# Performance work log

Hardware: AMD Instinct MI355X
Metric: run time of the kernel (lower is better)

## Reference

```python
import math
import jax, jax.numpy as jnp
import numpy as np

N_NODES = 50_000
N_EDGES = 500_000
INPUT_DIM = 6
HIDDEN = 128
FREQS = 32
LN_EPS = 1e-5
TWO_PI = 2.0 * math.pi


def wrap_angle(a):
    return (a + math.pi) % (2.0 * math.pi) - math.pi


def setup_inputs() -> dict:
    key = jax.random.key(0)
    ks = jax.random.split(key, 12)
    source = jax.random.normal(ks[0], (N_NODES, 5), dtype=jnp.float32)
    target = jax.random.normal(ks[1], (N_NODES, 5), dtype=jnp.float32)
    edge = jax.random.randint(ks[2], (2, N_EDGES), 0, N_NODES, dtype=jnp.int64)
    K = 2 * FREQS + 1
    # FourierEmbedding params: freqs table + 6 per-dim MLPs (Linear->LN->ReLU->Linear), stacked over dim axis
    freqs = jax.random.normal(ks[3], (INPUT_DIM, FREQS), dtype=jnp.float32)
    W1 = jax.random.normal(ks[4], (INPUT_DIM, K, HIDDEN), dtype=jnp.float32) * (1.0 / math.sqrt(K))
    b1 = jnp.zeros((INPUT_DIM, HIDDEN), dtype=jnp.float32)
    ln_w = jnp.ones((INPUT_DIM, HIDDEN), dtype=jnp.float32)
    ln_b = jnp.zeros((INPUT_DIM, HIDDEN), dtype=jnp.float32)
    W2 = jax.random.normal(ks[5], (INPUT_DIM, HIDDEN, HIDDEN), dtype=jnp.float32) * (1.0 / math.sqrt(HIDDEN))
    b2 = jnp.zeros((INPUT_DIM, HIDDEN), dtype=jnp.float32)
    return {"source": source, "target": target, "edge": edge,
            "freqs": freqs, "W1": W1, "b1": b1, "ln_w": ln_w, "ln_b": ln_b,
            "W2": W2, "b2": b2}


def _compute_feature(source, target, edge):
    # source/target: [N, 5] = X, Y, Heading, Speed, (other)
    sp, sh, ss = source[:, :2], source[:, 2], source[:, 3]
    tp, th, ts = target[:, :2], target[:, 2], target[:, 3]
    src, tgt = edge[0], edge[1]
    pd = sp[src] - tp[tgt]                         # [E, 2]
    dx, dy = pd[:, 0], pd[:, 1]
    dist = jnp.sqrt(dx * dx + dy * dy)
    is_close = (dist < 3.0).astype(pd.dtype)
    ang = jnp.arctan2(dy, dx)
    dh = wrap_angle(sh[src] - th[tgt])
    cos_a, sin_a = jnp.cos(ang), jnp.sin(ang)
    tvx, tvy = ts * jnp.cos(th), ts * jnp.sin(th)
    t_close = tvx[tgt] * cos_a + tvy[tgt] * sin_a
    svx, svy = ss * jnp.cos(sh), ss * jnp.sin(sh)
    s_close = svx[src] * cos_a + svy[src] * sin_a
    return jnp.stack([dx, dy, dh, is_close, t_close, s_close], axis=-1)  # [E, 6]


def _fourier_embed(feat, freqs, W1, b1, ln_w, ln_b, W2, b2):
    # feat: [E, 6]; freqs: [6, F]
    x = feat[:, :, None] * freqs[None, :, :] * TWO_PI          # [E, 6, F]
    x = jnp.concatenate([jnp.cos(x), jnp.sin(x), feat[:, :, None]], axis=-1)  # [E, 6, 2F+1]
    h = jnp.einsum('edk,dkh->edh', x, W1) + b1[None]           # [E, 6, H]
    mu = h.mean(axis=-1, keepdims=True)
    var = jnp.mean((h - mu) ** 2, axis=-1, keepdims=True)
    h = (h - mu) * jax.lax.rsqrt(var + LN_EPS) * ln_w[None] + ln_b[None]
    h = jax.nn.relu(h)
    out = jnp.einsum('edh,dhg->edg', h, W2) + b2[None]         # [E, 6, H]
    return out.sum(axis=1)                                     # [E, H]


def reference(source, target, edge, freqs, W1, b1, ln_w, ln_b, W2, b2):
    feat = jax.lax.stop_gradient(_compute_feature(source, target, edge))  # torch.no_grad()
    return _fourier_embed(feat, freqs, W1, b1, ln_w, ln_b, W2, b2)
```

## Files before the change

kernel.cpp:

```cpp
#include <hip/hip_runtime.h>
#include <hip/hip_bf16.h>
#include <math.h>

#define E_EDGES 500000
#define PI_F 3.14159265358979323846f
#define TWOPI_F 6.28318530717958647692f

typedef __attribute__((ext_vector_type(4))) float f32x4;
typedef __attribute__((ext_vector_type(8))) short s16x8;

static __device__ __forceinline__ short f2bf(float x) {
    __hip_bfloat16 h = __float2bfloat16(x);
    return __builtin_bit_cast(short, h);
}

__global__ void rape_prep_kernel(const float* __restrict__ W1,
                                 const float* __restrict__ W2,
                                 s16x8* __restrict__ ws)
{
    const int d  = blockIdx.x / 24;
    const int sg = blockIdx.x % 24;
    const int j  = threadIdx.x;
    s16x8 v;
    if (sg < 8) {
        const float* W1d = W1 + (size_t)d * 65 * 128;
        const int kb = (sg >> 2) * 32 + (sg & 3) * 4;
        #pragma unroll
        for (int i = 0; i < 4; ++i) {
            v[i]     = f2bf(W1d[(kb + i) * 128 + j]);
            v[i + 4] = f2bf(W1d[(kb + 16 + i) * 128 + j]);
        }
    } else {
        const int sg2 = sg - 8;
        const float* W2d = W2 + (size_t)d * 128 * 128;
        const int kb = (sg2 >> 2) * 32 + (sg2 & 3) * 4;
        #pragma unroll
        for (int i = 0; i < 4; ++i) {
            v[i]     = f2bf(W2d[(kb + i) * 128 + j]);
            v[i + 4] = f2bf(W2d[(kb + 16 + i) * 128 + j]);
        }
    }
    ws[(size_t)d * 24 * 128 + sg * 128 + j] = v;
}

__global__ __launch_bounds__(256, 2)
void rape_mfma5_kernel(const float* __restrict__ source,
                       const float* __restrict__ target,
                       const int*   __restrict__ edge,
                       const float* __restrict__ freqs,
                       const float* __restrict__ W1,
                       const float* __restrict__ b1,
                       const float* __restrict__ ln_w,
                       const float* __restrict__ ln_b,
                       const float* __restrict__ b2,
                       const s16x8* __restrict__ wsg,
                       float* __restrict__ out)
{
    __shared__ s16x8 slab[24 * 128];
    __shared__ float feat_s[6][128];
    __shared__ float b1_s[768];
    __shared__ float lnw_s[768];
    __shared__ float lnb_s[768];
    __shared__ float w164_s[768];
    __shared__ float freq_s[192];

    const int tid   = threadIdx.x;
    const int lane  = tid & 63;
    const int wv    = tid >> 6;
    const int c     = lane & 15;
    const int g     = lane >> 4;
    const int ebase = blockIdx.x * 128;

    for (int i = tid; i < 768; i += 256) {
        b1_s[i]   = b1[i];
        lnw_s[i]  = ln_w[i];
        lnb_s[i]  = ln_b[i];
        w164_s[i] = W1[((size_t)(i >> 7) * 65 + 64) * 128 + (i & 127)];
    }
    if (tid < 192) freq_s[tid] = freqs[tid];

    if (tid < 128) {
        int ec = ebase + tid; if (ec >= E_EDGES) ec = E_EDGES - 1;
        int si = edge[ec];
        int ti = edge[E_EDGES + ec];
        const float* S = source + (size_t)si * 5;
        const float* T = target + (size_t)ti * 5;
        float spx = S[0], spy = S[1], shd = S[2], ss = S[3];
        float tpx = T[0], tpy = T[1], thd = T[2], ts = T[3];
        float dx = spx - tpx, dy = spy - tpy;
        float dist = sqrtf(dx * dx + dy * dy);
        float ic  = dist < 3.0f ? 1.0f : 0.0f;
        float inv = dist > 0.0f ? 1.0f / dist : 0.0f;
        float ca  = dist > 0.0f ? dx * inv : 1.0f;
        float sa  = dy * inv;
        float a = shd - thd + PI_F;
        float r = fmodf(a, TWOPI_F);
        r = r < 0.0f ? r + TWOPI_F : r;
        float dh = r - PI_F;
        float tc = ts * (cosf(thd) * ca + sinf(thd) * sa);
        float sc = ss * (cosf(shd) * ca + sinf(shd) * sa);
        feat_s[0][tid] = dx; feat_s[1][tid] = dy; feat_s[2][tid] = dh;
        feat_s[3][tid] = ic; feat_s[4][tid] = tc; feat_s[5][tid] = sc;
    }

    f32x4 acc[2][8];
    #pragma unroll
    for (int gt = 0; gt < 8; ++gt) {
        f32x4 s = {0.f, 0.f, 0.f, 0.f};
        #pragma unroll
        for (int d = 0; d < 6; ++d)
            s += *(const f32x4*)(b2 + d * 128 + gt * 16 + g * 4);
        acc[0][gt] = s; acc[1][gt] = s;
    }

    for (int d = 0; d < 6; ++d) {
        __syncthreads();

        {
            const char* gsrc = (const char*)(wsg + (size_t)d * 24 * 128);
            #pragma unroll
            for (int it = 0; it < 12; ++it) {
                const int off = tid * 16 + it * 4096;
                __builtin_amdgcn_global_load_lds(
                    (const __attribute__((address_space(1))) unsigned int*)(gsrc + off),
                    (__attribute__((address_space(3))) unsigned int*)((char*)slab + off),
                    16, 0, 0);
            }
        }

        s16x8 bfr[2][2];
        float xv[2];
        const f32x4 fq0 = *(const f32x4*)(freq_s + d * 32 + g * 4);
        const f32x4 fq1 = *(const f32x4*)(freq_s + d * 32 + 16 + g * 4);
        #pragma unroll
        for (int es = 0; es < 2; ++es) {
            const float x = feat_s[d][wv * 32 + es * 16 + c];
            xv[es] = x;
            s16x8 bc, bs;
            #pragma unroll
            for (int i = 0; i < 8; ++i) {
                const float f = (i < 4) ? fq0[i] : fq1[i - 4];
                const float t = x * f;
                const float tf = t - floorf(t);
                bc[i] = f2bf(__builtin_amdgcn_cosf(tf));
                bs[i] = f2bf(__builtin_amdgcn_sinf(tf));
            }
            bfr[es][0] = bc; bfr[es][1] = bs;
        }

        f32x4 d1[2][8];
        #pragma unroll
        for (int jt = 0; jt < 8; ++jt) {
            const f32x4 bv  = *(const f32x4*)(b1_s   + d * 128 + jt * 16 + g * 4);
            const f32x4 wv4 = *(const f32x4*)(w164_s + d * 128 + jt * 16 + g * 4);
            d1[0][jt] = bv + xv[0] * wv4;
            d1[1][jt] = bv + xv[1] * wv4;
        }

        __syncthreads();

        #pragma unroll
        for (int jt = 0; jt < 8; ++jt) {
            const s16x8 a0 = slab[(0 + g) * 128 + jt * 16 + c];
            const s16x8 a1 = slab[(4 + g) * 128 + jt * 16 + c];
            #pragma unroll
            for (int es = 0; es < 2; ++es) {
                d1[es][jt] = __builtin_amdgcn_mfma_f32_16x16x32_bf16(a0, bfr[es][0], d1[es][jt], 0, 0, 0);
                d1[es][jt] = __builtin_amdgcn_mfma_f32_16x16x32_bf16(a1, bfr[es][1], d1[es][jt], 0, 0, 0);
            }
        }

        float mu[2], rinv[2];
        #pragma unroll
        for (int es = 0; es < 2; ++es) {
            float s1 = 0.f, s2 = 0.f;
            #pragma unroll
            for (int jt = 0; jt < 8; ++jt)
                #pragma unroll
                for (int q = 0; q < 4; ++q) {
                    const float v = d1[es][jt][q];
                    s1 += v; s2 = fmaf(v, v, s2);
                }
            s1 += __shfl_xor(s1, 16); s1 += __shfl_xor(s1, 32);
            s2 += __shfl_xor(s2, 16); s2 += __shfl_xor(s2, 32);
            mu[es] = s1 * 0.0078125f;
            const float var = s2 * 0.0078125f - mu[es] * mu[es];
            rinv[es] = rsqrtf(var + 1e-5f);
        }
        s16x8 pb[2][4];
        #pragma unroll
        for (int ks = 0; ks < 4; ++ks) {
            #pragma unroll
            for (int p = 0; p < 2; ++p) {
                const int jt = 2 * ks + p;
                const f32x4 lw = *(const f32x4*)(lnw_s + d * 128 + jt * 16 + g * 4);
                const f32x4 lb = *(const f32x4*)(lnb_s + d * 128 + jt * 16 + g * 4);
                #pragma unroll
                for (int es = 0; es < 2; ++es) {
                    #pragma unroll
                    for (int q = 0; q < 4; ++q) {
                        float hv = (d1[es][jt][q] - mu[es]) * rinv[es];
                        hv = fmaf(hv, lw[q], lb[q]);
                        hv = fmaxf(hv, 0.f);
                        pb[es][ks][q + 4 * p] = f2bf(hv);
                    }
                }
            }
        }

        #pragma unroll
        for (int gt = 0; gt < 8; ++gt) {
            const s16x8 a0 = slab[(8 + 0 * 4 + g) * 128 + gt * 16 + c];
            const s16x8 a1 = slab[(8 + 1 * 4 + g) * 128 + gt * 16 + c];
            const s16x8 a2 = slab[(8 + 2 * 4 + g) * 128 + gt * 16 + c];
            const s16x8 a3 = slab[(8 + 3 * 4 + g) * 128 + gt * 16 + c];
            #pragma unroll
            for (int es = 0; es < 2; ++es) {
                acc[es][gt] = __builtin_amdgcn_mfma_f32_16x16x32_bf16(a0, pb[es][0], acc[es][gt], 0, 0, 0);
                acc[es][gt] = __builtin_amdgcn_mfma_f32_16x16x32_bf16(a1, pb[es][1], acc[es][gt], 0, 0, 0);
                acc[es][gt] = __builtin_amdgcn_mfma_f32_16x16x32_bf16(a2, pb[es][2], acc[es][gt], 0, 0, 0);
                acc[es][gt] = __builtin_amdgcn_mfma_f32_16x16x32_bf16(a3, pb[es][3], acc[es][gt], 0, 0, 0);
            }
        }
    }

    #pragma unroll
    for (int es = 0; es < 2; ++es) {
        const int e = ebase + wv * 32 + es * 16 + c;
        if (e < E_EDGES) {
            float* op = out + (size_t)e * 128 + g * 4;
            #pragma unroll
            for (int gt = 0; gt < 8; ++gt)
                *(f32x4*)(op + gt * 16) = acc[es][gt];
        }
    }
}

extern "C" void kernel_launch(void* const* d_in, const int* in_sizes, int n_in,
                              void* d_out, int out_size, void* d_ws, size_t ws_size,
                              hipStream_t stream) {
    const float* source = (const float*)d_in[0];
    const float* target = (const float*)d_in[1];
    const int*   edge   = (const int*)  d_in[2];
    const float* freqs  = (const float*)d_in[3];
    const float* W1     = (const float*)d_in[4];
    const float* b1     = (const float*)d_in[5];
    const float* ln_w   = (const float*)d_in[6];
    const float* ln_b   = (const float*)d_in[7];
    const float* W2     = (const float*)d_in[8];
    const float* b2     = (const float*)d_in[9];
    float* out = (float*)d_out;
    s16x8* wsg = (s16x8*)d_ws;

    rape_prep_kernel<<<6 * 24, 128, 0, stream>>>(W1, W2, wsg);

    const int nblocks = (E_EDGES + 127) / 128;
    rape_mfma5_kernel<<<nblocks, 256, 0, stream>>>(
        source, target, edge, freqs, W1, b1, ln_w, ln_b, b2, wsg, out);
}
```

Baseline: 243.8 us.

## Raise edges per block to 192 and stream second GEMM per K-slice

Each wave now handles three 16-edge sub-tiles instead of two, so a block covers 192 edges. The per-dimension weight slab loaded into LDS is reused across more edges, and block count drops. The second GEMM is reorganised to build each K-slice of post-LayerNorm activations and consume it at once, cutting live registers to offset the larger accumulator array. Risks are higher register pressure at two blocks per CU, possible spills, and a longer feature-compute phase with more threads active.

```diff
diff --git a/kernel.cpp b/kernel.cpp
--- a/kernel.cpp
+++ b/kernel.cpp
@@ -5,6 +5,8 @@
 #define E_EDGES 500000
 #define PI_F 3.14159265358979323846f
 #define TWOPI_F 6.28318530717958647692f
+#define ES 3
+#define TE 192
 
 typedef __attribute__((ext_vector_type(4))) float f32x4;
 typedef __attribute__((ext_vector_type(8))) short s16x8;
@@ -44,7 +46,7 @@
 }
 
 __global__ __launch_bounds__(256, 2)
-void rape_mfma5_kernel(const float* __restrict__ source,
+void rape_mfma7_kernel(const float* __restrict__ source,
                        const float* __restrict__ target,
                        const int*   __restrict__ edge,
                        const float* __restrict__ freqs,
@@ -57,7 +59,7 @@
                        float* __restrict__ out)
 {
     __shared__ s16x8 slab[24 * 128];
-    __shared__ float feat_s[6][128];
+    __shared__ float feat_s[6][TE];
     __shared__ float b1_s[768];
     __shared__ float lnw_s[768];
     __shared__ float lnb_s[768];
@@ -69,7 +71,7 @@
     const int wv    = tid >> 6;
     const int c     = lane & 15;
     const int g     = lane >> 4;
-    const int ebase = blockIdx.x * 128;
+    const int ebase = blockIdx.x * TE;
 
     for (int i = tid; i < 768; i += 256) {
         b1_s[i]   = b1[i];
@@ -79,7 +81,7 @@
     }
     if (tid < 192) freq_s[tid] = freqs[tid];
 
-    if (tid < 128) {
+    if (tid < TE) {
         int ec = ebase + tid; if (ec >= E_EDGES) ec = E_EDGES - 1;
         int si = edge[ec];
         int ti = edge[E_EDGES + ec];
@@ -103,14 +105,15 @@
         feat_s[3][tid] = ic; feat_s[4][tid] = tc; feat_s[5][tid] = sc;
     }
 
-    f32x4 acc[2][8];
+    f32x4 acc[ES][8];
     #pragma unroll
     for (int gt = 0; gt < 8; ++gt) {
         f32x4 s = {0.f, 0.f, 0.f, 0.f};
         #pragma unroll
         for (int d = 0; d < 6; ++d)
             s += *(const f32x4*)(b2 + d * 128 + gt * 16 + g * 4);
-        acc[0][gt] = s; acc[1][gt] = s;
+        #pragma unroll
+        for (int es = 0; es < ES; ++es) acc[es][gt] = s;
     }
 
     for (int d = 0; d < 6; ++d) {
@@ -128,13 +131,13 @@
             }
         }
 
-        s16x8 bfr[2][2];
-        float xv[2];
+        s16x8 bfr[ES][2];
+        float xv[ES];
         const f32x4 fq0 = *(const f32x4*)(freq_s + d * 32 + g * 4);
         const f32x4 fq1 = *(const f32x4*)(freq_s + d * 32 + 16 + g * 4);
         #pragma unroll
-        for (int es = 0; es < 2; ++es) {
-            const float x = feat_s[d][wv * 32 + es * 16 + c];
+        for (int es = 0; es < ES; ++es) {
+            const float x = feat_s[d][wv * 48 + es * 16 + c];
             xv[es] = x;
             s16x8 bc, bs;
             #pragma unroll
@@ -148,13 +151,14 @@
             bfr[es][0] = bc; bfr[es][1] = bs;
         }
 
-        f32x4 d1[2][8];
+        f32x4 d1[ES][8];
         #pragma unroll
         for (int jt = 0; jt < 8; ++jt) {
             const f32x4 bv  = *(const f32x4*)(b1_s   + d * 128 + jt * 16 + g * 4);
             const f32x4 wv4 = *(const f32x4*)(w164_s + d * 128 + jt * 16 + g * 4);
-            d1[0][jt] = bv + xv[0] * wv4;
-            d1[1][jt] = bv + xv[1] * wv4;
+            #pragma unroll
+            for (int es = 0; es < ES; ++es)
+                d1[es][jt] = bv + xv[es] * wv4;
         }
 
         __syncthreads();
@@ -164,15 +168,15 @@
             const s16x8 a0 = slab[(0 + g) * 128 + jt * 16 + c];
             const s16x8 a1 = slab[(4 + g) * 128 + jt * 16 + c];
             #pragma unroll
-            for (int es = 0; es < 2; ++es) {
+            for (int es = 0; es < ES; ++es) {
                 d1[es][jt] = __builtin_amdgcn_mfma_f32_16x16x32_bf16(a0, bfr[es][0], d1[es][jt], 0, 0, 0);
                 d1[es][jt] = __builtin_amdgcn_mfma_f32_16x16x32_bf16(a1, bfr[es][1], d1[es][jt], 0, 0, 0);
             }
         }
 
-        float mu[2], rinv[2];
-        #pragma unroll
-        for (int es = 0; es < 2; ++es) {
+        float mu[ES], rinv[ES];
+        #pragma unroll
+        for (int es = 0; es < ES; ++es) {
             float s1 = 0.f, s2 = 0.f;
             #pragma unroll
             for (int jt = 0; jt < 8; ++jt)
@@ -187,46 +191,39 @@
             const float var = s2 * 0.0078125f - mu[es] * mu[es];
             rinv[es] = rsqrtf(var + 1e-5f);
         }
-        s16x8 pb[2][4];
+
         #pragma unroll
         for (int ks = 0; ks < 4; ++ks) {
+            s16x8 pbk[ES];
             #pragma unroll
             for (int p = 0; p < 2; ++p) {
                 const int jt = 2 * ks + p;
                 const f32x4 lw = *(const f32x4*)(lnw_s + d * 128 + jt * 16 + g * 4);
                 const f32x4 lb = *(const f32x4*)(lnb_s + d * 128 + jt * 16 + g * 4);
                 #pragma unroll
-                for (int es = 0; es < 2; ++es) {
+                for (int es = 0; es < ES; ++es) {
                     #pragma unroll
                     for (int q = 0; q < 4; ++q) {
                         float hv = (d1[es][jt][q] - mu[es]) * rinv[es];
                         hv = fmaf(hv, lw[q], lb[q]);
                         hv = fmaxf(hv, 0.f);
-                        pb[es][ks][q + 4 * p] = f2bf(hv);
+                        pbk[es][q + 4 * p] = f2bf(hv);
                     }
                 }
             }
-        }
-
-        #pragma unroll
-        for (int gt = 0; gt < 8; ++gt) {
-            const s16x8 a0 = slab[(8 + 0 * 4 + g) * 128 + gt * 16 + c];
-            const s16x8 a1 = slab[(8 + 1 * 4 + g) * 128 + gt * 16 + c];
-            const s16x8 a2 = slab[(8 + 2 * 4 + g) * 128 + gt * 16 + c];
-            const s16x8 a3 = slab[(8 + 3 * 4 + g) * 128 + gt * 16 + c];
-            #pragma unroll
-            for (int es = 0; es < 2; ++es) {
-                acc[es][gt] = __builtin_amdgcn_mfma_f32_16x16x32_bf16(a0, pb[es][0], acc[es][gt], 0, 0, 0);
-                acc[es][gt] = __builtin_amdgcn_mfma_f32_16x16x32_bf16(a1, pb[es][1], acc[es][gt], 0, 0, 0);
-                acc[es][gt] = __builtin_amdgcn_mfma_f32_16x16x32_bf16(a2, pb[es][2], acc[es][gt], 0, 0, 0);
-                acc[es][gt] = __builtin_amdgcn_mfma_f32_16x16x32_bf16(a3, pb[es][3], acc[es][gt], 0, 0, 0);
+            #pragma unroll
+            for (int gt = 0; gt < 8; ++gt) {
+                const s16x8 a = slab[(8 + ks * 4 + g) * 128 + gt * 16 + c];
+                #pragma unroll
+                for (int es = 0; es < ES; ++es)
+                    acc[es][gt] = __builtin_amdgcn_mfma_f32_16x16x32_bf16(a, pbk[es], acc[es][gt], 0, 0, 0);
             }
         }
     }
 
     #pragma unroll
-    for (int es = 0; es < 2; ++es) {
-        const int e = ebase + wv * 32 + es * 16 + c;
+    for (int es = 0; es < ES; ++es) {
+        const int e = ebase + wv * 48 + es * 16 + c;
         if (e < E_EDGES) {
             float* op = out + (size_t)e * 128 + g * 4;
             #pragma unroll
@@ -254,7 +251,7 @@
 
     rape_prep_kernel<<<6 * 24, 128, 0, stream>>>(W1, W2, wsg);
 
-    const int nblocks = (E_EDGES + 127) / 128;
-    rape_mfma5_kernel<<<nblocks, 256, 0, stream>>>(
+    const int nblocks = (E_EDGES + TE - 1) / TE;
+    rape_mfma7_kernel<<<nblocks, 256, 0, stream>>>(
         source, target, edge, freqs, W1, b1, ln_w, ln_b, b2, wsg, out);
 }
```

New measurement: 280.3 us. 15.0% more time.

## Split weight slab into two LDS buffers and raise occupancy to three blocks

Applied to the files above, without the earlier changes.

The per-dimension weight slab in LDS shrinks from 24 to 16 rows by staging it through two 8-row buffers. The second half of W2 is streamed into the first buffer while the first half of the W2 MFMAs runs from the second buffer. This lowers LDS use per block so that three blocks per CU can fit, and launch bounds are raised to match. In exchange it adds a barrier and a serialized load per dimension, and the tighter register budget at three blocks may cause spills.

```diff
diff --git a/kernel.cpp b/kernel.cpp
--- a/kernel.cpp
+++ b/kernel.cpp
@@ -43,20 +43,21 @@
     ws[(size_t)d * 24 * 128 + sg * 128 + j] = v;
 }
 
-__global__ __launch_bounds__(256, 2)
-void rape_mfma5_kernel(const float* __restrict__ source,
-                       const float* __restrict__ target,
-                       const int*   __restrict__ edge,
-                       const float* __restrict__ freqs,
-                       const float* __restrict__ W1,
-                       const float* __restrict__ b1,
-                       const float* __restrict__ ln_w,
-                       const float* __restrict__ ln_b,
-                       const float* __restrict__ b2,
-                       const s16x8* __restrict__ wsg,
-                       float* __restrict__ out)
+__global__ __launch_bounds__(256, 3)
+void rape_mfma10_kernel(const float* __restrict__ source,
+                        const float* __restrict__ target,
+                        const int*   __restrict__ edge,
+                        const float* __restrict__ freqs,
+                        const float* __restrict__ W1,
+                        const float* __restrict__ b1,
+                        const float* __restrict__ ln_w,
+                        const float* __restrict__ ln_b,
+                        const float* __restrict__ b2,
+                        const s16x8* __restrict__ wsg,
+                        float* __restrict__ out)
 {
-    __shared__ s16x8 slab[24 * 128];
+    __shared__ s16x8 slabA[8 * 128];
+    __shared__ s16x8 slabB[8 * 128];
     __shared__ float feat_s[6][128];
     __shared__ float b1_s[768];
     __shared__ float lnw_s[768];
@@ -119,11 +120,19 @@
         {
             const char* gsrc = (const char*)(wsg + (size_t)d * 24 * 128);
             #pragma unroll
-            for (int it = 0; it < 12; ++it) {
+            for (int it = 0; it < 4; ++it) {
                 const int off = tid * 16 + it * 4096;
                 __builtin_amdgcn_global_load_lds(
                     (const __attribute__((address_space(1))) unsigned int*)(gsrc + off),
-                    (__attribute__((address_space(3))) unsigned int*)((char*)slab + off),
+                    (__attribute__((address_space(3))) unsigned int*)((char*)slabA + off),
+                    16, 0, 0);
+            }
+            #pragma unroll
+            for (int it = 0; it < 4; ++it) {
+                const int off = tid * 16 + it * 4096;
+                __builtin_amdgcn_global_load_lds(
+                    (const __attribute__((address_space(1))) unsigned int*)(gsrc + 16384 + off),
+                    (__attribute__((address_space(3))) unsigned int*)((char*)slabB + off),
                     16, 0, 0);
             }
         }
@@ -161,8 +170,8 @@
 
         #pragma unroll
         for (int jt = 0; jt < 8; ++jt) {
-            const s16x8 a0 = slab[(0 + g) * 128 + jt * 16 + c];
-            const s16x8 a1 = slab[(4 + g) * 128 + jt * 16 + c];
+            const s16x8 a0 = slabA[(0 + g) * 128 + jt * 16 + c];
+            const s16x8 a1 = slabA[(4 + g) * 128 + jt * 16 + c];
             #pragma unroll
             for (int es = 0; es < 2; ++es) {
                 d1[es][jt] = __builtin_amdgcn_mfma_f32_16x16x32_bf16(a0, bfr[es][0], d1[es][jt], 0, 0, 0);
@@ -208,18 +217,41 @@
             }
         }
 
-        #pragma unroll
-        for (int gt = 0; gt < 8; ++gt) {
-            const s16x8 a0 = slab[(8 + 0 * 4 + g) * 128 + gt * 16 + c];
-            const s16x8 a1 = slab[(8 + 1 * 4 + g) * 128 + gt * 16 + c];
-            const s16x8 a2 = slab[(8 + 2 * 4 + g) * 128 + gt * 16 + c];
-            const s16x8 a3 = slab[(8 + 3 * 4 + g) * 128 + gt * 16 + c];
-            #pragma unroll
-            for (int es = 0; es < 2; ++es) {
-                acc[es][gt] = __builtin_amdgcn_mfma_f32_16x16x32_bf16(a0, pb[es][0], acc[es][gt], 0, 0, 0);
-                acc[es][gt] = __builtin_amdgcn_mfma_f32_16x16x32_bf16(a1, pb[es][1], acc[es][gt], 0, 0, 0);
-                acc[es][gt] = __builtin_amdgcn_mfma_f32_16x16x32_bf16(a2, pb[es][2], acc[es][gt], 0, 0, 0);
-                acc[es][gt] = __builtin_amdgcn_mfma_f32_16x16x32_bf16(a3, pb[es][3], acc[es][gt], 0, 0, 0);
+        __syncthreads();
+
+        {
+            const char* gsrc = (const char*)(wsg + (size_t)d * 24 * 128) + 32768;
+            #pragma unroll
+            for (int it = 0; it < 4; ++it) {
+                const int off = tid * 16 + it * 4096;
+                __builtin_amdgcn_global_load_lds(
+                    (const __attribute__((address_space(1))) unsigned int*)(gsrc + off),
+                    (__attribute__((address_space(3))) unsigned int*)((char*)slabA + off),
+                    16, 0, 0);
+            }
+        }
+
+        #pragma unroll
+        for (int ks = 0; ks < 2; ++ks) {
+            #pragma unroll
+            for (int gt = 0; gt < 8; ++gt) {
+                const s16x8 a = slabB[(ks * 4 + g) * 128 + gt * 16 + c];
+                #pragma unroll
+                for (int es = 0; es < 2; ++es)
+                    acc[es][gt] = __builtin_amdgcn_mfma_f32_16x16x32_bf16(a, pb[es][ks], acc[es][gt], 0, 0, 0);
+            }
+        }
+
+        __syncthreads();
+
+        #pragma unroll
+        for (int ks = 2; ks < 4; ++ks) {
+            #pragma unroll
+            for (int gt = 0; gt < 8; ++gt) {
+                const s16x8 a = slabA[((ks - 2) * 4 + g) * 128 + gt * 16 + c];
+                #pragma unroll
+                for (int es = 0; es < 2; ++es)
+                    acc[es][gt] = __builtin_amdgcn_mfma_f32_16x16x32_bf16(a, pb[es][ks], acc[es][gt], 0, 0, 0);
             }
         }
     }
@@ -255,6 +287,6 @@
     rape_prep_kernel<<<6 * 24, 128, 0, stream>>>(W1, W2, wsg);
 
     const int nblocks = (E_EDGES + 127) / 128;
-    rape_mfma5_kernel<<<nblocks, 256, 0, stream>>>(
+    rape_mfma10_kernel<<<nblocks, 256, 0, stream>>>(
         source, target, edge, freqs, W1, b1, ln_w, ln_b, b2, wsg, out);
 }
```

Result: slower. 284.5 us (+16.7%).
